# Optimization experiments

Hardware: AMD Instinct MI355X
Metric: run time of the kernel (lower is better)

The kernel has to match this reference:

```python
import jax, jax.numpy as jnp
import numpy as np

N = 50000      # nodes
E = 800000     # edges (avg degree 16)
IN = 128       # in_channels
OUT = 64       # out_channels (latent)
H = 2 * OUT    # hidden = 2*out_channels


def setup_inputs() -> dict:
    key = jax.random.key(0)
    ks = jax.random.split(key, 7)
    s = 0.1
    return {
        "x": jax.random.normal(ks[0], (N, IN), jnp.float32),
        "edge_index": jax.random.randint(ks[1], (2, E), 0, N, dtype=jnp.int64),
        "W1": jax.random.normal(ks[2], (IN, H), jnp.float32) * s,
        "b1": jnp.zeros((H,), jnp.float32),
        "Wmu": jax.random.normal(ks[3], (H, OUT), jnp.float32) * s,
        "bmu": jnp.zeros((OUT,), jnp.float32),
        "Wls": jax.random.normal(ks[4], (H, OUT), jnp.float32) * s,
        "bls": jnp.zeros((OUT,), jnp.float32),
        "eps": jax.random.normal(ks[5], (N, OUT), jnp.float32),
    }


def _gcn_conv(x, W, b, src, dst, dinv):
    # GCNConv: h = W x, out = D^-1/2 (A + I) D^-1/2 h + b
    h = x @ W                                   # [N, F]
    norm = (dinv[src] * dinv[dst])[:, None]     # [E, 1]
    agg = jax.ops.segment_sum(h[src] * norm, dst, num_segments=N)
    agg = agg + h * (dinv * dinv)[:, None]      # self-loop term
    return agg + b


def reference(x, edge_index, W1, b1, Wmu, bmu, Wls, bls, eps):
    src, dst = edge_index[0], edge_index[1]
    # degree with self-loops (PyG gcn_norm counts in-degree on dst/col)
    deg = jax.ops.segment_sum(jnp.ones((E,), x.dtype), dst, num_segments=N) + 1.0
    dinv = deg ** -0.5  # deg >= 1, safe

    h = jax.nn.relu(_gcn_conv(x, W1, b1, src, dst, dinv))
    mu = _gcn_conv(h, Wmu, bmu, src, dst, dinv)
    # Faithful to source bug: logstd also uses convmu weights
    logstd = _gcn_conv(h, Wmu, bmu, src, dst, dinv)
    # training-mode reparameterization with externally supplied noise
    zeta = mu + eps * jnp.exp(logstd)
    return (mu, logstd, zeta)
```

## Files before the change

kernel.cpp:

```cpp
#include <hip/hip_runtime.h>
#include <math.h>

#define N_NODES 50000
#define N_EDGES 800000
#define IN_C    128
#define H_C     128
#define OUT_C   64
#define BCAP    64
#define EPB     2048
#define CSTRIDE 16

typedef unsigned short u16;
typedef unsigned int   u32;

__device__ __forceinline__ u16 f2bf(float f) {
    u32 u; __builtin_memcpy(&u, &f, 4);
    u += 0x7FFFu + ((u >> 16) & 1u);
    return (u16)(u >> 16);
}
__device__ __forceinline__ float bflo(u32 p) { u32 u = p << 16;         float f; __builtin_memcpy(&f, &u, 4); return f; }
__device__ __forceinline__ float bfhi(u32 p) { u32 u = p & 0xFFFF0000u; float f; __builtin_memcpy(&f, &u, 4); return f; }

__global__ void k_detect_i64(const int* __restrict__ ei, int* __restrict__ flag) {
    int t = threadIdx.x;
    int nz = 0;
    for (int i = t; i < 256; i += 64)
        if (ei[2 * i + 1] != 0) nz = 1;
    unsigned long long b = __ballot(nz != 0);
    if (t == 0) *flag = (b == 0ULL) ? 1 : 0;
}

__device__ __forceinline__ int eidx(const int* __restrict__ ei, size_t pos, int mode) {
    return mode ? ei[pos << 1] : ei[pos];
}

__global__ void k_sort(const int* __restrict__ ei, const int* __restrict__ flag,
                       int* __restrict__ cursor, u16* __restrict__ sorted_src) {
    const int part  = blockIdx.x & 7;
    const int chunk = blockIdx.x >> 3;
    const int base  = chunk * EPB;
    const int m = *flag;
    for (int i = threadIdx.x; i < EPB; i += 256) {
        int e = base + i;
        if (e >= N_EDGES) break;
        int d = eidx(ei, (size_t)N_EDGES + e, m);
        if ((d & 7) != part) continue;
        int s = eidx(ei, (size_t)e, m);
        int c = atomicAdd(&cursor[(size_t)d << 4], 1);
        if (c < BCAP) sorted_src[((size_t)d << 6) + c] = (u16)s;
    }
}

__global__ void k_dinv(const int* __restrict__ cursor, float* __restrict__ dinv) {
    int i = blockIdx.x * blockDim.x + threadIdx.x;
    if (i < N_NODES) dinv[i] = rsqrtf((float)cursor[(size_t)i << 4] + 1.0f);
}

__launch_bounds__(512, 6)
__global__ void k_gemm1(const float* __restrict__ X, const float* __restrict__ W,
                        const float* __restrict__ dinv, u16* __restrict__ outq) {
    __shared__ __align__(16) char xs[32768];
    const int tid = threadIdx.x, wv = tid >> 6, lane = tid & 63;
    const int row0 = blockIdx.x * 64 + wv * 8;
    const size_t limit = (size_t)N_NODES * 512 - 1024;
    const char* Xb = (const char*)X;

#pragma unroll
    for (int chk = 0; chk < 4; ++chk) {
        size_t off = (size_t)row0 * 512 + (size_t)chk * 1024;
        if (off > limit) off = limit;
        __builtin_amdgcn_global_load_lds(
            (const __attribute__((address_space(1))) void*)(Xb + off + (size_t)lane * 16),
            (__attribute__((address_space(3))) void*)(xs + wv * 4096 + chk * 1024),
            16, 0, 0);
    }
    asm volatile("s_waitcnt vmcnt(0)" ::: "memory");
    __builtin_amdgcn_sched_barrier(0);

    const int c4 = (lane & 31) * 4;
    const int rs = lane >> 5;

    float4 acc[4];
#pragma unroll
    for (int r = 0; r < 4; ++r) acc[r] = make_float4(0.f, 0.f, 0.f, 0.f);

#pragma unroll 2
    for (int k4 = 0; k4 < IN_C / 4; ++k4) {
        float4 xv[4];
#pragma unroll
        for (int r = 0; r < 4; ++r)
            xv[r] = *reinterpret_cast<const float4*>(
                &xs[wv * 4096 + (rs + r * 2) * 512 + k4 * 16]);
        float4 w0 = *reinterpret_cast<const float4*>(W + (size_t)(4 * k4 + 0) * H_C + c4);
        float4 w1 = *reinterpret_cast<const float4*>(W + (size_t)(4 * k4 + 1) * H_C + c4);
        float4 w2 = *reinterpret_cast<const float4*>(W + (size_t)(4 * k4 + 2) * H_C + c4);
        float4 w3 = *reinterpret_cast<const float4*>(W + (size_t)(4 * k4 + 3) * H_C + c4);
#pragma unroll
        for (int r = 0; r < 4; ++r) {
            acc[r].x = fmaf(xv[r].x, w0.x, acc[r].x);
            acc[r].y = fmaf(xv[r].x, w0.y, acc[r].y);
            acc[r].z = fmaf(xv[r].x, w0.z, acc[r].z);
            acc[r].w = fmaf(xv[r].x, w0.w, acc[r].w);
            acc[r].x = fmaf(xv[r].y, w1.x, acc[r].x);
            acc[r].y = fmaf(xv[r].y, w1.y, acc[r].y);
            acc[r].z = fmaf(xv[r].y, w1.z, acc[r].z);
            acc[r].w = fmaf(xv[r].y, w1.w, acc[r].w);
            acc[r].x = fmaf(xv[r].z, w2.x, acc[r].x);
            acc[r].y = fmaf(xv[r].z, w2.y, acc[r].y);
            acc[r].z = fmaf(xv[r].z, w2.z, acc[r].z);
            acc[r].w = fmaf(xv[r].z, w2.w, acc[r].w);
            acc[r].x = fmaf(xv[r].w, w3.x, acc[r].x);
            acc[r].y = fmaf(xv[r].w, w3.y, acc[r].y);
            acc[r].z = fmaf(xv[r].w, w3.z, acc[r].z);
            acc[r].w = fmaf(xv[r].w, w3.w, acc[r].w);
        }
    }

#pragma unroll
    for (int r = 0; r < 4; ++r) {
        int row = row0 + rs + r * 2;
        if (row < N_NODES) {
            float di = dinv[row];
            ushort4 o;
            o.x = f2bf(acc[r].x * di);
            o.y = f2bf(acc[r].y * di);
            o.z = f2bf(acc[r].z * di);
            o.w = f2bf(acc[r].w * di);
            *reinterpret_cast<ushort4*>(outq + (size_t)row * H_C + c4) = o;
        }
    }
}

__launch_bounds__(256, 4)
__global__ void k_gemm2(const u16* __restrict__ gbuf, const float* __restrict__ W,
                        u16* __restrict__ outp) {
    __shared__ __align__(16) char xs[32768];
    const int tid = threadIdx.x, wv = tid >> 6, lane = tid & 63;
    const int row0 = blockIdx.x * 128 + wv * 32;
    const size_t limit = (size_t)N_NODES * 256 - 1024;
    const char* Gb = (const char*)gbuf;

#pragma unroll
    for (int chk = 0; chk < 8; ++chk) {
        size_t off = (size_t)row0 * 256 + (size_t)chk * 1024;
        if (off > limit) off = limit;
        __builtin_amdgcn_global_load_lds(
            (const __attribute__((address_space(1))) void*)(Gb + off + (size_t)lane * 16),
            (__attribute__((address_space(3))) void*)(xs + wv * 8192 + chk * 1024),
            16, 0, 0);
    }
    asm volatile("s_waitcnt vmcnt(0)" ::: "memory");
    __builtin_amdgcn_sched_barrier(0);

    const int c4 = (lane & 15) * 4;
    const int rs = lane >> 4;

    float4 acc[8];
#pragma unroll
    for (int r = 0; r < 8; ++r) acc[r] = make_float4(0.f, 0.f, 0.f, 0.f);

#pragma unroll 2
    for (int k4 = 0; k4 < IN_C / 4; ++k4) {
        float4 xv[8];
#pragma unroll
        for (int r = 0; r < 8; ++r) {
            int rl = rs + r * 4;
            uint2 u = *reinterpret_cast<const uint2*>(
                &xs[wv * 8192 + rl * 256 + k4 * 8]);
            xv[r].x = bflo(u.x); xv[r].y = bfhi(u.x);
            xv[r].z = bflo(u.y); xv[r].w = bfhi(u.y);
        }
        float4 w0 = *reinterpret_cast<const float4*>(W + (size_t)(4 * k4 + 0) * OUT_C + c4);
        float4 w1 = *reinterpret_cast<const float4*>(W + (size_t)(4 * k4 + 1) * OUT_C + c4);
        float4 w2 = *reinterpret_cast<const float4*>(W + (size_t)(4 * k4 + 2) * OUT_C + c4);
        float4 w3 = *reinterpret_cast<const float4*>(W + (size_t)(4 * k4 + 3) * OUT_C + c4);
#pragma unroll
        for (int r = 0; r < 8; ++r) {
            acc[r].x = fmaf(xv[r].x, w0.x, acc[r].x);
            acc[r].y = fmaf(xv[r].x, w0.y, acc[r].y);
            acc[r].z = fmaf(xv[r].x, w0.z, acc[r].z);
            acc[r].w = fmaf(xv[r].x, w0.w, acc[r].w);
            acc[r].x = fmaf(xv[r].y, w1.x, acc[r].x);
            acc[r].y = fmaf(xv[r].y, w1.y, acc[r].y);
            acc[r].z = fmaf(xv[r].y, w1.z, acc[r].z);
            acc[r].w = fmaf(xv[r].y, w1.w, acc[r].w);
            acc[r].x = fmaf(xv[r].z, w2.x, acc[r].x);
            acc[r].y = fmaf(xv[r].z, w2.y, acc[r].y);
            acc[r].z = fmaf(xv[r].z, w2.z, acc[r].z);
            acc[r].w = fmaf(xv[r].z, w2.w, acc[r].w);
            acc[r].x = fmaf(xv[r].w, w3.x, acc[r].x);
            acc[r].y = fmaf(xv[r].w, w3.y, acc[r].y);
            acc[r].z = fmaf(xv[r].w, w3.z, acc[r].z);
            acc[r].w = fmaf(xv[r].w, w3.w, acc[r].w);
        }
    }

#pragma unroll
    for (int r = 0; r < 8; ++r) {
        int row = row0 + rs + r * 4;
        if (row < N_NODES) {
            ushort4 o;
            o.x = f2bf(acc[r].x);
            o.y = f2bf(acc[r].y);
            o.z = f2bf(acc[r].z);
            o.w = f2bf(acc[r].w);
            *reinterpret_cast<ushort4*>(outp + (size_t)row * OUT_C + c4) = o;
        }
    }
}

template <int C, int MODE>
__global__ void k_agg(const u16* __restrict__ sorted_src,
                      const int* __restrict__ cursor,
                      const float* __restrict__ dinv,
                      const u16* __restrict__ rows,
                      const float* __restrict__ bias,
                      const float* __restrict__ eps,
                      void* __restrict__ outbuf) {
    const int wave = threadIdx.x >> 6;
    const int lane = threadIdx.x & 63;
    const int n = blockIdx.x * 4 + wave;
    if (n >= N_NODES) return;

    int c = cursor[(size_t)n << 4]; if (c > BCAP) c = BCAP;
    const int beg = n << 6;
    const int end = beg + c;
    const float di = dinv[n];

    if (C == 128) {
        const u32* rw = reinterpret_cast<const u32*>(rows);
        const int pi = lane;
        float a0 = 0.f, a1 = 0.f, b0 = 0.f, b1 = 0.f;
        int j = beg;
        for (; j + 8 <= end; j += 8) {
            ushort4 sa = *reinterpret_cast<const ushort4*>(sorted_src + j);
            ushort4 sb = *reinterpret_cast<const ushort4*>(sorted_src + j + 4);
            u32 p0 = rw[(size_t)sa.x * 64 + pi];
            u32 p1 = rw[(size_t)sa.y * 64 + pi];
            u32 p2 = rw[(size_t)sa.z * 64 + pi];
            u32 p3 = rw[(size_t)sa.w * 64 + pi];
            u32 p4 = rw[(size_t)sb.x * 64 + pi];
            u32 p5 = rw[(size_t)sb.y * 64 + pi];
            u32 p6 = rw[(size_t)sb.z * 64 + pi];
            u32 p7 = rw[(size_t)sb.w * 64 + pi];
            a0 += bflo(p0) + bflo(p2);  a1 += bfhi(p0) + bfhi(p2);
            b0 += bflo(p1) + bflo(p3);  b1 += bfhi(p1) + bfhi(p3);
            a0 += bflo(p4) + bflo(p6);  a1 += bfhi(p4) + bfhi(p6);
            b0 += bflo(p5) + bflo(p7);  b1 += bfhi(p5) + bfhi(p7);
        }
        for (; j + 4 <= end; j += 4) {
            ushort4 sa = *reinterpret_cast<const ushort4*>(sorted_src + j);
            u32 p0 = rw[(size_t)sa.x * 64 + pi];
            u32 p1 = rw[(size_t)sa.y * 64 + pi];
            u32 p2 = rw[(size_t)sa.z * 64 + pi];
            u32 p3 = rw[(size_t)sa.w * 64 + pi];
            a0 += bflo(p0) + bflo(p2);  a1 += bfhi(p0) + bfhi(p2);
            b0 += bflo(p1) + bflo(p3);  b1 += bfhi(p1) + bfhi(p3);
        }
        for (; j < end; ++j) {
            u32 p0 = rw[(size_t)sorted_src[j] * 64 + pi];
            a0 += bflo(p0); a1 += bfhi(p0);
        }
        u32 qn = rw[(size_t)n * 64 + pi];
        const int c0 = lane * 2;
        float px = fmaf(di, a0 + b0 + bflo(qn), bias[c0]);
        float py = fmaf(di, a1 + b1 + bfhi(qn), bias[c0 + 1]);
        ushort2 o;
        o.x = f2bf(di * fmaxf(px, 0.f));
        o.y = f2bf(di * fmaxf(py, 0.f));
        *reinterpret_cast<ushort2*>((u16*)outbuf + (size_t)n * 128 + c0) = o;
    } else {
        float a0 = 0.f, a1 = 0.f, b0 = 0.f, b1 = 0.f;
        int j = beg;
        for (; j + 8 <= end; j += 8) {
            ushort4 sa = *reinterpret_cast<const ushort4*>(sorted_src + j);
            ushort4 sb = *reinterpret_cast<const ushort4*>(sorted_src + j + 4);
            float f0, f1, f2, f3, f4, f5, f6, f7;
            { u32 u = (u32)rows[(size_t)sa.x * 64 + lane] << 16; __builtin_memcpy(&f0, &u, 4); }
            { u32 u = (u32)rows[(size_t)sa.y * 64 + lane] << 16; __builtin_memcpy(&f1, &u, 4); }
            { u32 u = (u32)rows[(size_t)sa.z * 64 + lane] << 16; __builtin_memcpy(&f2, &u, 4); }
            { u32 u = (u32)rows[(size_t)sa.w * 64 + lane] << 16; __builtin_memcpy(&f3, &u, 4); }
            { u32 u = (u32)rows[(size_t)sb.x * 64 + lane] << 16; __builtin_memcpy(&f4, &u, 4); }
            { u32 u = (u32)rows[(size_t)sb.y * 64 + lane] << 16; __builtin_memcpy(&f5, &u, 4); }
            { u32 u = (u32)rows[(size_t)sb.z * 64 + lane] << 16; __builtin_memcpy(&f6, &u, 4); }
            { u32 u = (u32)rows[(size_t)sb.w * 64 + lane] << 16; __builtin_memcpy(&f7, &u, 4); }
            a0 += f0 + f2;  a1 += f1 + f3;
            b0 += f4 + f6;  b1 += f5 + f7;
        }
        for (; j + 4 <= end; j += 4) {
            ushort4 sa = *reinterpret_cast<const ushort4*>(sorted_src + j);
            float f0, f1, f2, f3;
            { u32 u = (u32)rows[(size_t)sa.x * 64 + lane] << 16; __builtin_memcpy(&f0, &u, 4); }
            { u32 u = (u32)rows[(size_t)sa.y * 64 + lane] << 16; __builtin_memcpy(&f1, &u, 4); }
            { u32 u = (u32)rows[(size_t)sa.z * 64 + lane] << 16; __builtin_memcpy(&f2, &u, 4); }
            { u32 u = (u32)rows[(size_t)sa.w * 64 + lane] << 16; __builtin_memcpy(&f3, &u, 4); }
            a0 += f0 + f2;  a1 += f1 + f3;
        }
        for (; j < end; ++j) {
            u32 u = (u32)rows[(size_t)sorted_src[j] * 64 + lane] << 16;
            float f; __builtin_memcpy(&f, &u, 4);
            a0 += f;
        }
        float pn;
        { u32 u = (u32)rows[(size_t)n * 64 + lane] << 16; __builtin_memcpy(&pn, &u, 4); }
        float* out = (float*)outbuf;
        float m = fmaf(di, (a0 + a1) + (b0 + b1) + pn, bias[lane]);
        const int NM = N_NODES * OUT_C;
        int i = n * 64 + lane;
        float z = fmaf(eps[i], expf(m), m);
        out[i]          = m;
        out[NM + i]     = m;
        out[2 * NM + i] = z;
    }
}

extern "C" void kernel_launch(void* const* d_in, const int* in_sizes, int n_in,
                              void* d_out, int out_size, void* d_ws, size_t ws_size,
                              hipStream_t stream) {
    const float* x   = (const float*)d_in[0];
    const int*   ei  = (const int*)d_in[1];
    const float* W1  = (const float*)d_in[2];
    const float* b1  = (const float*)d_in[3];
    const float* Wmu = (const float*)d_in[4];
    const float* bmu = (const float*)d_in[5];
    const float* eps = (const float*)d_in[8];
    float* out = (float*)d_out;

    char* p = (char*)d_ws;
    int*  flag   = (int*)p;                        p += 16;
    int*  cursor = (int*)p;                        p += (size_t)N_NODES * CSTRIDE * 4;
    float* dinv  = (float*)p;                      p += ((size_t)N_NODES * 4 + 15) / 16 * 16;
    u16* sorted  = (u16*)p;                        p += ((size_t)N_NODES * BCAP * 2 + 15) / 16 * 16;
    u16* bufA    = (u16*)p;                        p += ((size_t)N_NODES * H_C * 2 + 15) / 16 * 16;
    u16* bufG    = (u16*)p;
    u16* bufP    = bufA;

    hipMemsetAsync(cursor, 0, (size_t)N_NODES * CSTRIDE * sizeof(int), stream);
    k_detect_i64<<<1, 64, 0, stream>>>(ei, flag);
    k_sort<<<8 * ((N_EDGES + EPB - 1) / EPB), 256, 0, stream>>>(ei, flag, cursor, sorted);
    k_dinv<<<(N_NODES + 255) / 256, 256, 0, stream>>>(cursor, dinv);

    k_gemm1<<<(N_NODES + 63) / 64, 512, 0, stream>>>(x, W1, dinv, bufA);
    k_agg<H_C, 0><<<(N_NODES + 3) / 4, 256, 0, stream>>>(sorted, cursor, dinv, bufA, b1, nullptr, bufG);
    k_gemm2<<<(N_NODES + 127) / 128, 256, 0, stream>>>(bufG, Wmu, bufP);
    k_agg<OUT_C, 1><<<(N_NODES + 3) / 4, 256, 0, stream>>>(sorted, cursor, dinv, bufP, bmu, eps, out);
}
```

Baseline: 183.0 us.

## Stage bf16 W1 in LDS for gemm1 and compact per-node edge counts

Adds a kernel that converts W1 to bf16. gemm1 now copies the whole bf16 weight matrix into shared memory with async global-to-LDS loads and reads weights from LDS instead of global memory. This doubles LDS use per block and lowers the launch-bounds occupancy hint. k_dinv also writes a clamped uint8 count per node, so the aggregation kernels read one byte instead of a strided int from the padded cursor array. The risks are a small precision loss from bf16 weights and one extra kernel launch.

```diff
diff --git a/kernel.cpp b/kernel.cpp
--- a/kernel.cpp
+++ b/kernel.cpp
@@ -10,6 +10,7 @@
 #define EPB     2048
 #define CSTRIDE 16
 
+typedef unsigned char  u8;
 typedef unsigned short u16;
 typedef unsigned int   u32;
 
@@ -32,6 +33,11 @@
 
 __device__ __forceinline__ int eidx(const int* __restrict__ ei, size_t pos, int mode) {
     return mode ? ei[pos << 1] : ei[pos];
+}
+
+__global__ void k_wcvt(const float* __restrict__ W, u16* __restrict__ Wbf) {
+    int i = blockIdx.x * 256 + threadIdx.x;
+    if (i < IN_C * H_C) Wbf[i] = f2bf(W[i]);
 }
 
 __global__ void k_sort(const int* __restrict__ ei, const int* __restrict__ flag,
@@ -51,19 +57,25 @@
     }
 }
 
-__global__ void k_dinv(const int* __restrict__ cursor, float* __restrict__ dinv) {
+__global__ void k_dinv(const int* __restrict__ cursor, float* __restrict__ dinv,
+                       u8* __restrict__ cnt8) {
     int i = blockIdx.x * blockDim.x + threadIdx.x;
-    if (i < N_NODES) dinv[i] = rsqrtf((float)cursor[(size_t)i << 4] + 1.0f);
-}
-
-__launch_bounds__(512, 6)
-__global__ void k_gemm1(const float* __restrict__ X, const float* __restrict__ W,
+    if (i < N_NODES) {
+        int c = cursor[(size_t)i << 4];
+        dinv[i] = rsqrtf((float)c + 1.0f);
+        cnt8[i] = (u8)(c > BCAP ? BCAP : c);
+    }
+}
+
+__launch_bounds__(512, 4)
+__global__ void k_gemm1(const float* __restrict__ X, const u16* __restrict__ Wbf,
                         const float* __restrict__ dinv, u16* __restrict__ outq) {
-    __shared__ __align__(16) char xs[32768];
+    __shared__ __align__(16) char lds[65536];
     const int tid = threadIdx.x, wv = tid >> 6, lane = tid & 63;
     const int row0 = blockIdx.x * 64 + wv * 8;
     const size_t limit = (size_t)N_NODES * 512 - 1024;
     const char* Xb = (const char*)X;
+    const char* Wb = (const char*)Wbf;
 
 #pragma unroll
     for (int chk = 0; chk < 4; ++chk) {
@@ -71,11 +83,19 @@
         if (off > limit) off = limit;
         __builtin_amdgcn_global_load_lds(
             (const __attribute__((address_space(1))) void*)(Xb + off + (size_t)lane * 16),
-            (__attribute__((address_space(3))) void*)(xs + wv * 4096 + chk * 1024),
+            (__attribute__((address_space(3))) void*)(lds + wv * 4096 + chk * 1024),
             16, 0, 0);
     }
+#pragma unroll
+    for (int chk = 0; chk < 4; ++chk) {
+        int wc = wv * 4 + chk;
+        __builtin_amdgcn_global_load_lds(
+            (const __attribute__((address_space(1))) void*)(Wb + (size_t)wc * 1024 + (size_t)lane * 16),
+            (__attribute__((address_space(3))) void*)(lds + 32768 + wc * 1024),
+            16, 0, 0);
+    }
     asm volatile("s_waitcnt vmcnt(0)" ::: "memory");
-    __builtin_amdgcn_sched_barrier(0);
+    __syncthreads();
 
     const int c4 = (lane & 31) * 4;
     const int rs = lane >> 5;
@@ -90,29 +110,33 @@
 #pragma unroll
         for (int r = 0; r < 4; ++r)
             xv[r] = *reinterpret_cast<const float4*>(
-                &xs[wv * 4096 + (rs + r * 2) * 512 + k4 * 16]);
-        float4 w0 = *reinterpret_cast<const float4*>(W + (size_t)(4 * k4 + 0) * H_C + c4);
-        float4 w1 = *reinterpret_cast<const float4*>(W + (size_t)(4 * k4 + 1) * H_C + c4);
-        float4 w2 = *reinterpret_cast<const float4*>(W + (size_t)(4 * k4 + 2) * H_C + c4);
-        float4 w3 = *reinterpret_cast<const float4*>(W + (size_t)(4 * k4 + 3) * H_C + c4);
+                &lds[wv * 4096 + (rs + r * 2) * 512 + k4 * 16]);
+        float4 w[4];
 #pragma unroll
         for (int r = 0; r < 4; ++r) {
-            acc[r].x = fmaf(xv[r].x, w0.x, acc[r].x);
-            acc[r].y = fmaf(xv[r].x, w0.y, acc[r].y);
-            acc[r].z = fmaf(xv[r].x, w0.z, acc[r].z);
-            acc[r].w = fmaf(xv[r].x, w0.w, acc[r].w);
-            acc[r].x = fmaf(xv[r].y, w1.x, acc[r].x);
-            acc[r].y = fmaf(xv[r].y, w1.y, acc[r].y);
-            acc[r].z = fmaf(xv[r].y, w1.z, acc[r].z);
-            acc[r].w = fmaf(xv[r].y, w1.w, acc[r].w);
-            acc[r].x = fmaf(xv[r].z, w2.x, acc[r].x);
-            acc[r].y = fmaf(xv[r].z, w2.y, acc[r].y);
-            acc[r].z = fmaf(xv[r].z, w2.z, acc[r].z);
-            acc[r].w = fmaf(xv[r].z, w2.w, acc[r].w);
-            acc[r].x = fmaf(xv[r].w, w3.x, acc[r].x);
-            acc[r].y = fmaf(xv[r].w, w3.y, acc[r].y);
-            acc[r].z = fmaf(xv[r].w, w3.z, acc[r].z);
-            acc[r].w = fmaf(xv[r].w, w3.w, acc[r].w);
+            uint2 wu = *reinterpret_cast<const uint2*>(
+                &lds[32768 + (4 * k4 + r) * 256 + (lane & 31) * 8]);
+            w[r].x = bflo(wu.x); w[r].y = bfhi(wu.x);
+            w[r].z = bflo(wu.y); w[r].w = bfhi(wu.y);
+        }
+#pragma unroll
+        for (int r = 0; r < 4; ++r) {
+            acc[r].x = fmaf(xv[r].x, w[0].x, acc[r].x);
+            acc[r].y = fmaf(xv[r].x, w[0].y, acc[r].y);
+            acc[r].z = fmaf(xv[r].x, w[0].z, acc[r].z);
+            acc[r].w = fmaf(xv[r].x, w[0].w, acc[r].w);
+            acc[r].x = fmaf(xv[r].y, w[1].x, acc[r].x);
+            acc[r].y = fmaf(xv[r].y, w[1].y, acc[r].y);
+            acc[r].z = fmaf(xv[r].y, w[1].z, acc[r].z);
+            acc[r].w = fmaf(xv[r].y, w[1].w, acc[r].w);
+            acc[r].x = fmaf(xv[r].z, w[2].x, acc[r].x);
+            acc[r].y = fmaf(xv[r].z, w[2].y, acc[r].y);
+            acc[r].z = fmaf(xv[r].z, w[2].z, acc[r].z);
+            acc[r].w = fmaf(xv[r].z, w[2].w, acc[r].w);
+            acc[r].x = fmaf(xv[r].w, w[3].x, acc[r].x);
+            acc[r].y = fmaf(xv[r].w, w[3].y, acc[r].y);
+            acc[r].z = fmaf(xv[r].w, w[3].z, acc[r].z);
+            acc[r].w = fmaf(xv[r].w, w[3].w, acc[r].w);
         }
     }
 
@@ -211,7 +235,7 @@
 
 template <int C, int MODE>
 __global__ void k_agg(const u16* __restrict__ sorted_src,
-                      const int* __restrict__ cursor,
+                      const u8* __restrict__ cnt8,
                       const float* __restrict__ dinv,
                       const u16* __restrict__ rows,
                       const float* __restrict__ bias,
@@ -222,7 +246,7 @@
     const int n = blockIdx.x * 4 + wave;
     if (n >= N_NODES) return;
 
-    int c = cursor[(size_t)n << 4]; if (c > BCAP) c = BCAP;
+    const int c = cnt8[n];
     const int beg = n << 6;
     const int end = beg + c;
     const float di = dinv[n];
@@ -330,6 +354,8 @@
     int*  flag   = (int*)p;                        p += 16;
     int*  cursor = (int*)p;                        p += (size_t)N_NODES * CSTRIDE * 4;
     float* dinv  = (float*)p;                      p += ((size_t)N_NODES * 4 + 15) / 16 * 16;
+    u8*  cnt8    = (u8*)p;                         p += ((size_t)N_NODES + 15) / 16 * 16;
+    u16* wbf     = (u16*)p;                        p += (size_t)IN_C * H_C * 2;
     u16* sorted  = (u16*)p;                        p += ((size_t)N_NODES * BCAP * 2 + 15) / 16 * 16;
     u16* bufA    = (u16*)p;                        p += ((size_t)N_NODES * H_C * 2 + 15) / 16 * 16;
     u16* bufG    = (u16*)p;
@@ -337,11 +363,12 @@
 
     hipMemsetAsync(cursor, 0, (size_t)N_NODES * CSTRIDE * sizeof(int), stream);
     k_detect_i64<<<1, 64, 0, stream>>>(ei, flag);
+    k_wcvt<<<(IN_C * H_C + 255) / 256, 256, 0, stream>>>(W1, wbf);
     k_sort<<<8 * ((N_EDGES + EPB - 1) / EPB), 256, 0, stream>>>(ei, flag, cursor, sorted);
-    k_dinv<<<(N_NODES + 255) / 256, 256, 0, stream>>>(cursor, dinv);
-
-    k_gemm1<<<(N_NODES + 63) / 64, 512, 0, stream>>>(x, W1, dinv, bufA);
-    k_agg<H_C, 0><<<(N_NODES + 3) / 4, 256, 0, stream>>>(sorted, cursor, dinv, bufA, b1, nullptr, bufG);
+    k_dinv<<<(N_NODES + 255) / 256, 256, 0, stream>>>(cursor, dinv, cnt8);
+
+    k_gemm1<<<(N_NODES + 63) / 64, 512, 0, stream>>>(x, wbf, dinv, bufA);
+    k_agg<H_C, 0><<<(N_NODES + 3) / 4, 256, 0, stream>>>(sorted, cnt8, dinv, bufA, b1, nullptr, bufG);
     k_gemm2<<<(N_NODES + 127) / 128, 256, 0, stream>>>(bufG, Wmu, bufP);
-    k_agg<OUT_C, 1><<<(N_NODES + 3) / 4, 256, 0, stream>>>(sorted, cursor, dinv, bufP, bmu, eps, out);
-}
+    k_agg<OUT_C, 1><<<(N_NODES + 3) / 4, 256, 0, stream>>>(sorted, cnt8, dinv, bufP, bmu, eps, out);
+}
```

Result: faster. 178.8 us (-2.3%).
